# Kernel optimization log

Hardware: AMD Instinct MI355X
Metric: run time of the kernel (lower is better)

## Reference

```python
import math
import jax, jax.numpy as jnp
import numpy as np

L_LAYERS, H, D, DV, DM, LMAX, V = 4, 16, 1024, 64, 4096, 1024, 32000


def setup_inputs() -> dict:
    key = jax.random.key(0)
    ks = iter(jax.random.split(key, 40))
    def rn(shape, s=0.02):
        return jax.random.normal(next(ks), shape, jnp.float32) * s
    x_ids = jax.random.randint(next(ks), (LMAX,), 0, V)
    return dict(
        x_ids=x_ids,
        word_emb=rn((V, D)), pos_emb=rn((LMAX, D)),
        Wq=rn((L_LAYERS, H, D, D)), bq=jnp.zeros((L_LAYERS, H, D), jnp.float32),
        Wk=rn((L_LAYERS, H, D, D)), bk=jnp.zeros((L_LAYERS, H, D), jnp.float32),
        Wv=rn((L_LAYERS, H, D, DV)), bv=jnp.zeros((L_LAYERS, H, DV), jnp.float32),
        Wo=rn((L_LAYERS, H * DV, D)), bo=jnp.zeros((L_LAYERS, D), jnp.float32),
        g1=rn((L_LAYERS, D), 0.01), b1=rn((L_LAYERS, D), 0.01),
        g2=rn((L_LAYERS, D), 0.01), b2=rn((L_LAYERS, D), 0.01),
        W1=rn((L_LAYERS, D, DM)), bm1=jnp.zeros((L_LAYERS, DM), jnp.float32),
        W2=rn((L_LAYERS, DM, D)), bm2=jnp.zeros((L_LAYERS, D), jnp.float32),
        gf=rn((D,), 0.01), bf=rn((D,), 0.01),
        Wu=rn((D, V)), bu=jnp.zeros((V,), jnp.float32),
    )


def _ln(x, g, b):
    # original normalizes each row over the full embedding vector (biased std)
    mu = jnp.mean(x, axis=-1, keepdims=True)
    sd = jnp.sqrt(jnp.mean((x - mu) ** 2, axis=-1, keepdims=True))
    return g * (x - mu) / sd + b


def reference(x_ids, word_emb, pos_emb, Wq, bq, Wk, bk, Wv, bv, Wo, bo,
              g1, b1, g2, b2, W1, bm1, W2, bm2, gf, bf, Wu, bu):
    x = word_emb[x_ids] + pos_emb[jnp.arange(LMAX)]          # (LMAX, D)
    mask = jnp.tril(jnp.ones((LMAX, LMAX), bool))
    scale = 1.0 / math.sqrt(D)                               # d_attn = d_e
    for l in range(L_LAYERS):
        xn = _ln(x, g1[l], b1[l])
        q = jnp.einsum('ld,hde->hle', xn, Wq[l]) + bq[l][:, None, :]
        k = jnp.einsum('ld,hde->hle', xn, Wk[l]) + bk[l][:, None, :]
        v = jnp.einsum('ld,hdv->hlv', xn, Wv[l]) + bv[l][:, None, :]
        s = jnp.einsum('hqe,hke->hqk', q, k)                 # (H, LMAX, LMAX)
        s = jnp.where(mask, s, -jnp.inf)
        a = jax.nn.softmax(s * scale, axis=-1)
        o = jnp.einsum('hqk,hkv->hqv', a, v)                 # (H, LMAX, DV)
        # faithful reproduction of MHAttention's OVERLAPPING slice writes:
        # head h writes columns [h, h+DV), later heads overwrite earlier ones
        y = jnp.zeros((LMAX, H * DV), x.dtype)
        for h in range(H):
            y = y.at[:, h:h + DV].set(o[h])
        x = x + y @ Wo[l] + bo[l]
        xn2 = _ln(x, g2[l], b2[l])
        # x + act_layer(xn2) where act_layer(z) = z + mlp2(gelu(mlp1(z)))
        x = x + xn2 + jax.nn.gelu(xn2 @ W1[l] + bm1[l]) @ W2[l] + bm2[l]
    x = _ln(x, gf, bf)
    return jax.nn.softmax(x @ Wu + bu, axis=-1)              # (LMAX, V)
```

## Files before the change

### kernel.cpp

```cpp
#include <hip/hip_runtime.h>

typedef __bf16 bf16_t;
typedef __bf16 bf16x8 __attribute__((ext_vector_type(8)));
typedef float f32x4 __attribute__((ext_vector_type(4)));
typedef unsigned int u32;

#define SEQ    1024
#define DEMB   1024
#define NHEAD  16
#define DVDIM  64
#define DMLP   4096
#define NVOCAB 32000
#define NLAYER 4

typedef const __attribute__((address_space(1))) void gas_t;
typedef __attribute__((address_space(3))) void las_t;

__device__ __forceinline__ void gload_lds16(const void* g, void* l) {
  __builtin_amdgcn_global_load_lds((gas_t*)g, (las_t*)l, 16, 0, 0);
}

union PackU { bf16_t h[2]; u32 u; };
union B4U  { uint2 u; bf16_t h[4]; };

__device__ __forceinline__ float blockSum(float v, float* red) {
  #pragma unroll
  for (int o = 32; o > 0; o >>= 1) v += __shfl_down(v, o, 64);
  __syncthreads();
  if ((threadIdx.x & 63) == 0) red[threadIdx.x >> 6] = v;
  __syncthreads();
  return (red[0] + red[1]) + (red[2] + red[3]);
}
__device__ __forceinline__ float blockMax(float v, float* red) {
  #pragma unroll
  for (int o = 32; o > 0; o >>= 1) v = fmaxf(v, __shfl_down(v, o, 64));
  __syncthreads();
  if ((threadIdx.x & 63) == 0) red[threadIdx.x >> 6] = v;
  __syncthreads();
  return fmaxf(fmaxf(red[0], red[1]), fmaxf(red[2], red[3]));
}

__device__ __forceinline__ void ln_body(float4 v, const float* __restrict__ g,
                                        const float* __restrict__ b,
                                        bf16_t* __restrict__ xn, int row, int t,
                                        float* red, float* xupd_row) {
  float mu = blockSum(v.x + v.y + v.z + v.w, red) * (1.0f / DEMB);
  float dx = v.x - mu, dy = v.y - mu, dz = v.z - mu, dw = v.w - mu;
  float var = blockSum(dx * dx + dy * dy + dz * dz + dw * dw, red) * (1.0f / DEMB);
  float inv = 1.0f / sqrtf(var);
  float4 gv = *(const float4*)(g + t * 4);
  float4 bv = *(const float4*)(b + t * 4);
  float o0 = gv.x * dx * inv + bv.x;
  float o1 = gv.y * dy * inv + bv.y;
  float o2 = gv.z * dz * inv + bv.z;
  float o3 = gv.w * dw * inv + bv.w;
  PackU p0, p1;
  p0.h[0] = (bf16_t)o0; p0.h[1] = (bf16_t)o1;
  p1.h[0] = (bf16_t)o2; p1.h[1] = (bf16_t)o3;
  uint2 st; st.x = p0.u; st.y = p1.u;
  *(uint2*)(xn + (long)row * DEMB + t * 4) = st;
  if (xupd_row) {
    float4 nv; nv.x = v.x + o0; nv.y = v.y + o1; nv.z = v.z + o2; nv.w = v.w + o3;
    *(float4*)(xupd_row + t * 4) = nv;
  }
}

__global__ void __launch_bounds__(256)
embedln_k(const int* __restrict__ ids, const float* __restrict__ we,
          const float* __restrict__ pe, const float* __restrict__ g,
          const float* __restrict__ b, float* __restrict__ x,
          bf16_t* __restrict__ xn) {
  __shared__ float red[4];
  const int row = blockIdx.x, t = threadIdx.x;
  const long id = ids[row];
  float4 a = *(const float4*)(we + id * (long)DEMB + t * 4);
  float4 p = *(const float4*)(pe + (long)row * DEMB + t * 4);
  float4 v; v.x = a.x + p.x; v.y = a.y + p.y; v.z = a.z + p.z; v.w = a.w + p.w;
  *(float4*)(x + (long)row * DEMB + t * 4) = v;
  ln_body(v, g, b, xn, row, t, red, nullptr);
}

__global__ void __launch_bounds__(256)
ln_k(const float* __restrict__ x, const float* __restrict__ g,
     const float* __restrict__ b, bf16_t* __restrict__ xn,
     float* __restrict__ xupd) {
  __shared__ float red[4];
  const int row = blockIdx.x, t = threadIdx.x;
  float4 v = *(const float4*)(x + (long)row * DEMB + t * 4);
  ln_body(v, g, b, xn, row, t, red, xupd ? xupd + (long)row * DEMB : nullptr);
}

__global__ void __launch_bounds__(256)
redln_k(const float* __restrict__ P, const float* __restrict__ bm2,
        float* __restrict__ X, const float* __restrict__ g,
        const float* __restrict__ b, bf16_t* __restrict__ xn) {
  __shared__ float red[4];
  const int row = blockIdx.x, t = threadIdx.x;
  const long i = (long)row * 1024 + t * 4;
  float4 x = *(float4*)(X + i);
  #pragma unroll
  for (int z = 0; z < 4; ++z) {
    float4 p = *(const float4*)(P + (long)z * 1048576 + i);
    x.x += p.x; x.y += p.y; x.z += p.z; x.w += p.w;
  }
  float4 bb = *(const float4*)(bm2 + t * 4);
  x.x += bb.x; x.y += bb.y; x.z += bb.z; x.w += bb.w;
  *(float4*)(X + i) = x;
  ln_body(x, g, b, xn, row, t, red, nullptr);
}

__global__ void biaszyb_k(const float* __restrict__ bq, const float* __restrict__ bk,
                          float* __restrict__ out, bf16_t* __restrict__ y) {
  const int z = blockIdx.x, t = threadIdx.x;
  if (z < 128) {
    const int l = z >> 5, i = z & 31;
    const float* src = (i < NHEAD) ? (bq + (long)(l * NHEAD + i) * DEMB)
                                   : (bk + (long)(l * NHEAD + i - NHEAD) * DEMB);
    *(float4*)(out + (long)z * DEMB + t * 4) = *(const float4*)(src + t * 4);
  } else {
    *(uint4*)((char*)y + ((long)(z - 128) * 256 + t) * 16) = uint4{0, 0, 0, 0};
  }
}

__device__ __forceinline__ void tconv_tile(const float* __restrict__ ip,
                                           bf16_t* __restrict__ op,
                                           int R, int C, int rx, int ry,
                                           float (*tf)[65]) {
  const int c0 = rx * 64, r0 = ry * 64;
  const int t = threadIdx.x;
  const int lr = t >> 4, lc = (t & 15) * 4;
  #pragma unroll
  for (int p = 0; p < 4; ++p) {
    const float4 v = *(const float4*)(ip + (long)(r0 + lr + 16 * p) * C + (c0 + lc));
    tf[lr + 16 * p][lc + 0] = v.x;
    tf[lr + 16 * p][lc + 1] = v.y;
    tf[lr + 16 * p][lc + 2] = v.z;
    tf[lr + 16 * p][lc + 3] = v.w;
  }
  __syncthreads();
  const int j = t & 7;
  const int n = t >> 3;
  #pragma unroll
  for (int p = 0; p < 2; ++p) {
    const int nn = n + 32 * p;
    u32 w[4];
    #pragma unroll
    for (int q = 0; q < 4; ++q) {
      PackU u;
      u.h[0] = (bf16_t)tf[j * 8 + 2 * q][nn];
      u.h[1] = (bf16_t)tf[j * 8 + 2 * q + 1][nn];
      w[q] = u.u;
    }
    *(uint4*)(op + (long)(c0 + nn) * R + (r0 + j * 8)) = *(uint4*)&w[0];
  }
}

__global__ void __launch_bounds__(256)
tconvall_k(const float* __restrict__ Wq, const float* __restrict__ Wk,
           const float* __restrict__ Wv, const float* __restrict__ Wo,
           const float* __restrict__ W1, const float* __restrict__ W2,
           const float* __restrict__ Wu,
           bf16_t* __restrict__ WTqk, bf16_t* __restrict__ WTv,
           bf16_t* __restrict__ WTo, bf16_t* __restrict__ WT1,
           bf16_t* __restrict__ WT2, bf16_t* __restrict__ WTu) {
  __shared__ float tf[64][65];
  const long DD = (long)DEMB * DEMB;
  const int b = blockIdx.x;
  const float* ip; bf16_t* op; int R, C, rx, ry;
  if (b < 32768) {
    const int z = b >> 8, rem = b & 255; ry = rem >> 4; rx = rem & 15;
    R = 1024; C = 1024;
    const int l = z >> 5, i = z & 31;
    ip = (i < NHEAD) ? (Wq + (long)(l * NHEAD + i) * DD)
                     : (Wk + (long)(l * NHEAD + i - NHEAD) * DD);
    op = WTqk + (long)z * DD;
  } else if (b < 33792) {
    const int idx = b - 32768; const int z = idx >> 4; ry = idx & 15; rx = 0;
    R = 1024; C = 64;
    ip = Wv + (long)z * 65536; op = WTv + (long)z * 65536;
  } else if (b < 33920) {
    const int idx = b - 33792; const int z = idx >> 5; ry = (idx >> 4) & 1; rx = idx & 15;
    R = 128; C = 1024;
    ip = Wo + (long)z * DD; op = WTo + (long)z * 131072;
  } else if (b < 38016) {
    const int idx = b - 33920; const int z = idx >> 10; ry = (idx >> 6) & 15; rx = idx & 63;
    R = 1024; C = 4096;
    ip = W1 + (long)z * 4194304; op = WT1 + (long)z * 4194304;
  } else if (b < 42112) {
    const int idx = b - 38016; const int z = idx >> 10; ry = (idx >> 4) & 63; rx = idx & 15;
    R = 4096; C = 1024;
    ip = W2 + (long)z * 4194304; op = WT2 + (long)z * 4194304;
  } else {
    const int idx = b - 42112; ry = idx / 500; rx = idx - ry * 500;
    R = 1024; C = 32000;
    ip = Wu; op = WTu;
  }
  tconv_tile(ip, op, R, C, rx, ry, tf);
}

template<int MODE, int BN, bool CAUSAL, bool TRIMK>
__global__ void __launch_bounds__(256)
gemm_k(const bf16_t* __restrict__ A, const bf16_t* __restrict__ B,
       const float* __restrict__ bias, void* __restrict__ Cv,
       int M, int N, int K, int lda, int ldb,
       long aB, long bB, long cB, int biasB) {
  __shared__ bf16_t lsA[128 * 32];
  __shared__ bf16_t lsB[BN * 32];

  const int t = threadIdx.x;
  const int bz = blockIdx.z;
  const int m0 = blockIdx.y * 128;
  const int n0 = blockIdx.x * BN;
  if (CAUSAL && n0 > m0 + 127) return;

  const bf16_t* Ap = A + (long)bz * aB;
  const bf16_t* Bp = B + (long)bz * bB;
  const int kEnd = TRIMK ? min(K, m0 + 128) : K;

  constexpr int NS = BN / 32;
  const int lane = t & 63;
  const int wid = t >> 6;
  const int wr = (wid >> 1) * 64;
  const int wc = (wid & 1) * (BN / 2);
  const int fr = lane & 15, fg = lane >> 4;
  const int srow = lane >> 2;
  const int skc  = (lane & 3) * 8;

  f32x4 acc[4][NS] = {};

  for (int k0 = 0; k0 < kEnd; k0 += 32) {
    if (k0) __syncthreads();
    #pragma unroll
    for (int i = 0; i < 2; ++i) {
      const int seg = wid * 2 + i;
      gload_lds16(Ap + (long)(m0 + seg * 16 + srow) * lda + (k0 + skc),
                  lsA + seg * 512);
    }
    if (BN == 128) {
      #pragma unroll
      for (int i = 0; i < 2; ++i) {
        const int seg = wid * 2 + i;
        gload_lds16(Bp + (long)(n0 + seg * 16 + srow) * ldb + (k0 + skc),
                    lsB + seg * 512);
      }
    } else {
      gload_lds16(Bp + (long)(n0 + wid * 16 + srow) * ldb + (k0 + skc),
                  lsB + wid * 512);
    }
    __syncthreads();

    bf16x8 af[4], bfv[NS];
    #pragma unroll
    for (int ms = 0; ms < 4; ++ms)
      af[ms] = *(const bf16x8*)(lsA + (wr + ms * 16 + fr) * 32 + fg * 8);
    #pragma unroll
    for (int ns = 0; ns < NS; ++ns)
      bfv[ns] = *(const bf16x8*)(lsB + (wc + ns * 16 + fr) * 32 + fg * 8);
    #pragma unroll
    for (int ms = 0; ms < 4; ++ms)
      #pragma unroll
      for (int ns = 0; ns < NS; ++ns)
        acc[ms][ns] = __builtin_amdgcn_mfma_f32_16x16x32_bf16(
            af[ms], bfv[ns], acc[ms][ns], 0, 0, 0);
  }

  #pragma unroll
  for (int ms = 0; ms < 4; ++ms) {
    #pragma unroll
    for (int ns = 0; ns < NS; ++ns) {
      const int col = n0 + wc + ns * 16 + fr;
      const float bvv = bias ? bias[(long)bz * biasB + col] : 0.0f;
      #pragma unroll
      for (int r = 0; r < 4; ++r) {
        const int row = m0 + wr + ms * 16 + fg * 4 + r;
        float v = acc[ms][ns][r] + bvv;
        if (MODE == 1) {
          ((float*)Cv)[(long)bz * cB + (long)row * N + col] += v;
        } else if (MODE == 2) {
          ((float*)Cv)[(long)bz * cB + (long)row * N + col] = v;
        } else if (MODE == 3) {
          float gl = 0.5f * v * (1.0f + tanhf(0.7978845608028654f * (v + 0.044715f * v * v * v)));
          ((bf16_t*)Cv)[(long)bz * cB + (long)row * N + col] = (bf16_t)gl;
        } else {
          ((bf16_t*)Cv)[(long)row * 128 + 15 + col] = (bf16_t)v;
        }
      }
    }
  }
}

#define GPHASE(buf, mh, nh, STAGE, VM) do {                                            \
  bf16x8 af[4][2], bfv[2][2];                                                          \
  _Pragma("unroll") for (int mf = 0; mf < 4; ++mf) {                                   \
    const int r = wm * 128 + ((mh) * 4 + mf) * 16 + (lane & 15);                       \
    _Pragma("unroll") for (int ks = 0; ks < 2; ++ks) {                                 \
      const int slot = ks * 4 + (lane >> 4);                                           \
      af[mf][ks] = *(const bf16x8*)(lds + (buf) * 32768 + r * 64 +                     \
                                    ((slot ^ (r & 7)) << 3)); } }                      \
  _Pragma("unroll") for (int nf = 0; nf < 2; ++nf) {                                   \
    const int r = wn * 64 + ((nh) * 2 + nf) * 16 + (lane & 15);                        \
    _Pragma("unroll") for (int ks = 0; ks < 2; ++ks) {                                 \
      const int slot = ks * 4 + (lane >> 4);                                           \
      bfv[nf][ks] = *(const bf16x8*)(lds + (buf) * 32768 + 16384 + r * 64 +            \
                                     ((slot ^ (r & 7)) << 3)); } }                     \
  STAGE;                                                                               \
  __builtin_amdgcn_s_barrier();                                                        \
  asm volatile("s_waitcnt lgkmcnt(0)" ::: "memory");                                   \
  __builtin_amdgcn_sched_barrier(0);                                                   \
  __builtin_amdgcn_s_setprio(1);                                                       \
  _Pragma("unroll") for (int mf = 0; mf < 4; ++mf)                                     \
    _Pragma("unroll") for (int nf = 0; nf < 2; ++nf)                                   \
      _Pragma("unroll") for (int ks = 0; ks < 2; ++ks)                                 \
        acc[(mh) * 4 + mf][(nh) * 2 + nf] = __builtin_amdgcn_mfma_f32_16x16x32_bf16(   \
            af[mf][ks], bfv[nf][ks], acc[(mh) * 4 + mf][(nh) * 2 + nf], 0, 0, 0);      \
  __builtin_amdgcn_s_setprio(0);                                                       \
  VM;                                                                                  \
  __builtin_amdgcn_s_barrier();                                                        \
} while (0)

template<int MODE, bool CAUSAL, bool HASV>
__global__ void __launch_bounds__(512, 1)
gemm256_k(const bf16_t* __restrict__ A, const bf16_t* __restrict__ B,
          const float* __restrict__ bias, void* __restrict__ Cv,
          int M, int N, int K, long aB, long bB, long cB, int biasB,
          const bf16_t* __restrict__ B2, const float* __restrict__ bias2,
          bf16_t* __restrict__ Cv2) {
  __shared__ bf16_t lds[65536];

  const int t = threadIdx.x;
  const int lane = t & 63, w = t >> 6;
  const int wm = w >> 2, wn = w & 3;
  const int bz = blockIdx.z;
  const int m0 = blockIdx.y * 256, n0 = blockIdx.x * 256;
  if (CAUSAL && n0 > m0 + 255) return;

  const bool vm = HASV && (bz == 32);
  const bf16_t* Ap = A + (long)bz * aB;
  const bf16_t* Bp = vm ? B2 : B + (long)bz * bB;
  const int NT = K >> 6;

  f32x4 acc[8][4] = {};

  auto stA = [&](int half, int kt, int buf) {
    #pragma unroll
    for (int rr = 0; rr < 2; ++rr) {
      const int rw0 = rr * 64 + w * 8;
      const int row0 = ((rw0 >> 6) << 7) | (half << 6) | (rw0 & 63);
      const int r = row0 + (lane >> 3);
      const int slot = lane & 7;
      gload_lds16(Ap + (long)(m0 + r) * K + (kt << 6) + ((slot ^ (r & 7)) << 3),
                  lds + buf * 32768 + row0 * 64);
    }
  };
  auto stB = [&](int half, int kt, int buf) {
    #pragma unroll
    for (int rr = 0; rr < 2; ++rr) {
      const int rw0 = rr * 64 + w * 8;
      const int row0 = ((rw0 >> 5) << 6) | (half << 5) | (rw0 & 31);
      const int r = row0 + (lane >> 3);
      const int slot = lane & 7;
      gload_lds16(Bp + (long)(n0 + r) * K + (kt << 6) + ((slot ^ (r & 7)) << 3),
                  lds + buf * 32768 + 16384 + row0 * 64);
    }
  };

  stB(0, 0, 0); stA(0, 0, 0); stA(1, 0, 0); stB(1, 0, 0);
  stB(0, 1, 1); stA(0, 1, 1);
  asm volatile("s_waitcnt vmcnt(4)" ::: "memory");
  __builtin_amdgcn_s_barrier();

  for (int it = 0; it < (NT >> 1); ++it) {
    const int tt = it * 2;
    const int s1 = min(tt + 1, NT - 1);
    const int s2 = min(tt + 2, NT - 1);
    const int s3 = min(tt + 3, NT - 1);
    GPHASE(0, 0, 0, { stA(1, s1, 1); }, );
    GPHASE(0, 1, 0, { stB(1, s1, 1); }, );
    GPHASE(0, 0, 1, { stB(0, s2, 0); }, );
    GPHASE(0, 1, 1, { stA(0, s2, 0); }, asm volatile("s_waitcnt vmcnt(4)" ::: "memory"));
    GPHASE(1, 0, 0, { stA(1, s2, 0); }, );
    GPHASE(1, 1, 0, { stB(1, s2, 0); }, );
    GPHASE(1, 0, 1, { stB(0, s3, 1); }, );
    GPHASE(1, 1, 1, { stA(0, s3, 1); }, asm volatile("s_waitcnt vmcnt(4)" ::: "memory"));
  }
  asm volatile("s_waitcnt vmcnt(0)" ::: "memory");

  #pragma unroll
  for (int mf = 0; mf < 8; ++mf) {
    #pragma unroll
    for (int nf = 0; nf < 4; ++nf) {
      const int col = n0 + wn * 64 + nf * 16 + (lane & 15);
      const int row0 = m0 + wm * 128 + mf * 16 + (lane >> 4) * 4;
      if (HASV && vm) {
        const float bvv = bias2[col];
        PackU p0, p1;
        p0.h[0] = (bf16_t)(acc[mf][nf][0] + bvv);
        p0.h[1] = (bf16_t)(acc[mf][nf][1] + bvv);
        p1.h[0] = (bf16_t)(acc[mf][nf][2] + bvv);
        p1.h[1] = (bf16_t)(acc[mf][nf][3] + bvv);
        uint2 st; st.x = p0.u; st.y = p1.u;
        *(uint2*)(Cv2 + (long)col * M + row0) = st;
      } else {
        const float bvv = bias ? bias[(long)bz * biasB + col] : 0.0f;
        #pragma unroll
        for (int r = 0; r < 4; ++r) {
          const float v = acc[mf][nf][r] + bvv;
          if (MODE == 0)
            ((bf16_t*)Cv)[(long)bz * cB + (long)(row0 + r) * N + col] = (bf16_t)v;
          else
            ((float*)Cv)[(long)bz * cB + (long)(row0 + r) * N + col] = v;
        }
      }
    }
  }
}

__global__ void __launch_bounds__(256)
smax_k(bf16_t* __restrict__ s, const bf16_t* __restrict__ V,
       bf16_t* __restrict__ Yb) {
  __shared__ float red[4];
  const int q = blockIdx.x, h = blockIdx.y, t = threadIdx.x;
  bf16_t* sr = s + ((long)h * SEQ + q) * SEQ;
  const int L = q + 1;
  const float scale = 0.03125f;
  B4U b; b.u = *(const uint2*)(sr + t * 4);
  float x[4];
  float m = -1e30f;
  #pragma unroll
  for (int j = 0; j < 4; ++j) {
    x[j] = (float)b.h[j] * scale;
    if (t * 4 + j < L) m = fmaxf(m, x[j]);
  }
  m = blockMax(m, red);
  float e[4], sum = 0.0f;
  #pragma unroll
  for (int j = 0; j < 4; ++j) {
    e[j] = (t * 4 + j < L) ? expf(x[j] - m) : 0.0f;
    sum += e[j];
  }
  __syncthreads();
  sum = blockSum(sum, red);
  const float inv = 1.0f / sum;
  #pragma unroll
  for (int j = 0; j < 4; ++j) b.h[j] = (bf16_t)(e[j] * inv);
  *(uint2*)(sr + t * 4) = b.u;
  if (h != NHEAD - 1) {
    const bf16_t* vc = V + (long)h * 64 * SEQ;
    B4U vv; vv.u = *(const uint2*)(vc + t * 4);
    float d = 0.0f;
    #pragma unroll
    for (int j = 0; j < 4; ++j) d += e[j] * (float)vv.h[j];
    d = blockSum(d, red);
    if (t == 0) Yb[(long)q * 128 + h] = (bf16_t)(d * inv);
  }
}

__global__ void __launch_bounds__(1024)
vsmax_k(float* __restrict__ out) {
  __shared__ float rm[16], rs[16];
  const int row = blockIdx.x, t = threadIdx.x;
  float* r = out + (long)row * NVOCAB;
  float v[32];
  const int nlast = (t < NVOCAB - 31 * 1024) ? 32 : 31;
  float m = -1e30f;
  #pragma unroll
  for (int j = 0; j < 31; ++j) { v[j] = r[j * 1024 + t]; m = fmaxf(m, v[j]); }
  if (nlast == 32) { v[31] = r[31 * 1024 + t]; m = fmaxf(m, v[31]); } else v[31] = -1e30f;
  float s = 0.0f;
  #pragma unroll
  for (int j = 0; j < 32; ++j) s += expf(v[j] - m);
  #pragma unroll
  for (int o = 32; o > 0; o >>= 1) {
    const float mo = __shfl_down(m, o, 64);
    const float so = __shfl_down(s, o, 64);
    const float M2 = fmaxf(m, mo);
    s = s * expf(m - M2) + so * expf(mo - M2);
    m = M2;
  }
  if ((t & 63) == 0) { rm[t >> 6] = m; rs[t >> 6] = s; }
  __syncthreads();
  float M = -1e30f;
  #pragma unroll
  for (int i = 0; i < 16; ++i) M = fmaxf(M, rm[i]);
  float S = 0.0f;
  #pragma unroll
  for (int i = 0; i < 16; ++i) S += rs[i] * expf(rm[i] - M);
  const float inv = 1.0f / S;
  #pragma unroll
  for (int j = 0; j < 31; ++j) r[j * 1024 + t] = expf(v[j] - M) * inv;
  if (nlast == 32) r[31 * 1024 + t] = expf(v[31] - M) * inv;
}

extern "C" void kernel_launch(void* const* d_in, const int* in_sizes, int n_in,
                              void* d_out, int out_size, void* d_ws, size_t ws_size,
                              hipStream_t stream) {
  (void)in_sizes; (void)n_in; (void)out_size; (void)ws_size;
  const int*   x_ids = (const int*)  d_in[0];
  const float* wemb  = (const float*)d_in[1];
  const float* pemb  = (const float*)d_in[2];
  const float* Wq    = (const float*)d_in[3];
  const float* bq    = (const float*)d_in[4];
  const float* Wk    = (const float*)d_in[5];
  const float* bk    = (const float*)d_in[6];
  const float* Wv    = (const float*)d_in[7];
  const float* bv    = (const float*)d_in[8];
  const float* Wo    = (const float*)d_in[9];
  const float* bo    = (const float*)d_in[10];
  const float* g1    = (const float*)d_in[11];
  const float* b1    = (const float*)d_in[12];
  const float* g2    = (const float*)d_in[13];
  const float* b2    = (const float*)d_in[14];
  const float* W1    = (const float*)d_in[15];
  const float* bm1   = (const float*)d_in[16];
  const float* W2    = (const float*)d_in[17];
  const float* bm2   = (const float*)d_in[18];
  const float* gf    = (const float*)d_in[19];
  const float* bfin  = (const float*)d_in[20];
  const float* Wu    = (const float*)d_in[21];
  const float* bu    = (const float*)d_in[22];

  char* ws = (char*)d_ws;
  float*  X    = (float*) ws;
  bf16_t* ACT  = (bf16_t*)(ws + (4u   << 20));
  bf16_t* VbT  = (bf16_t*)(ws + (6u   << 20));
  bf16_t* Yb   = (bf16_t*)(ws + (10u  << 20));
  bf16_t* H1   = (bf16_t*)(ws + (12u  << 20));
  bf16_t* QKb  = (bf16_t*)(ws + (20u  << 20));
  float*  PART = (float*) (ws + (84u  << 20));
  float*  BIAS = (float*) (ws + (100u << 20));
  bf16_t* WTqk = (bf16_t*)(ws + (128u << 20));
  bf16_t* WTv  = (bf16_t*)(ws + (384u << 20));
  bf16_t* WTo  = (bf16_t*)(ws + (392u << 20));
  bf16_t* WT1  = (bf16_t*)(ws + (400u << 20));
  bf16_t* WT2  = (bf16_t*)(ws + (432u << 20));
  bf16_t* WTu  = (bf16_t*)(ws + (464u << 20));

  bf16_t* Sb  = (bf16_t*)d_out;
  float*  OUT = (float*)d_out;

  const long DD = (long)DEMB * DEMB;
  const long SD = (long)SEQ * DEMB;

  embedln_k<<<SEQ, 256, 0, stream>>>(x_ids, wemb, pemb, g1, b1, X, ACT);
  biaszyb_k<<<192, 256, 0, stream>>>(bq, bk, BIAS, Yb);
  tconvall_k<<<50112, 256, 0, stream>>>(Wq, Wk, Wv, Wo, W1, W2, Wu,
                                        WTqk, WTv, WTo, WT1, WT2, WTu);

  for (int l = 0; l < NLAYER; ++l) {
    gemm256_k<0, false, true><<<dim3(4, 4, 33), 512, 0, stream>>>(
        ACT, WTqk + (long)l * 32 * DD, BIAS + (long)l * 32 * DEMB, QKb,
        SEQ, DEMB, DEMB, 0L, DD, SD, DEMB,
        WTv + (long)l * DD, bv + (long)l * NHEAD * DVDIM, VbT);

    gemm256_k<0, true, false><<<dim3(4, 4, NHEAD), 512, 0, stream>>>(
        QKb, QKb + (long)NHEAD * SD, nullptr, Sb,
        SEQ, SEQ, DEMB, SD, SD, (long)SEQ * SEQ, 0, nullptr, nullptr, nullptr);
    smax_k<<<dim3(SEQ, NHEAD), 256, 0, stream>>>(Sb, VbT, Yb);
    gemm_k<7, 64, false, true><<<dim3(1, 8, 1), 256, 0, stream>>>(
        Sb + (long)(NHEAD - 1) * SEQ * SEQ, VbT + (long)(NHEAD - 1) * DVDIM * SEQ,
        nullptr, Yb, SEQ, DVDIM, SEQ, SEQ, SEQ, 0L, 0L, 0L, 0);

    gemm_k<1, 64, false, false><<<dim3(16, 8, 1), 256, 0, stream>>>(
        Yb, WTo + (long)l * DEMB * 128, bo + (long)l * DEMB, X,
        SEQ, DEMB, 128, 128, 128, 0L, 0L, 0L, 0);

    ln_k<<<SEQ, 256, 0, stream>>>(X, g2 + l * DEMB, b2 + l * DEMB, ACT, X);

    gemm_k<3, 128, false, false><<<dim3(32, 8, 1), 256, 0, stream>>>(
        ACT, WT1 + (long)l * DMLP * DEMB, bm1 + (long)l * DMLP, H1,
        SEQ, DMLP, DEMB, DEMB, DEMB, 0L, 0L, 0L, 0);
    gemm_k<2, 128, false, false><<<dim3(8, 8, 4), 256, 0, stream>>>(
        H1, WT2 + (long)l * DEMB * DMLP, nullptr, PART,
        SEQ, DEMB, 1024, DMLP, DMLP, 1024L, 1024L, (long)SEQ * DEMB, 0);
    if (l < NLAYER - 1)
      redln_k<<<SEQ, 256, 0, stream>>>(PART, bm2 + (long)l * DEMB, X,
                                       g1 + (l + 1) * DEMB, b1 + (l + 1) * DEMB, ACT);
    else
      redln_k<<<SEQ, 256, 0, stream>>>(PART, bm2 + (long)l * DEMB, X, gf, bfin, ACT);
  }

  gemm256_k<2, false, false><<<dim3(125, 4, 1), 512, 0, stream>>>(
      ACT, WTu, bu, OUT, SEQ, NVOCAB, DEMB, 0L, 0L, 0L, 0,
      nullptr, nullptr, nullptr);
  vsmax_k<<<SEQ, 1024, 0, stream>>>(OUT);
}
```

Before: 1.510 ms.

## Fold last-head PV into softmax and move V projection into score GEMM

The V projection moves out of the QK projection GEMM and becomes an extra z-slice of the causal score GEMM, which fills idle blocks left by the causal skip. The last head's full P·V product, previously a separate small GEMM, is now computed inside the softmax kernel using LDS-staged probabilities, and the normalized probabilities are no longer written back to the score buffer. This removes one kernel launch and a large write of softmax output, at the cost of a heavier per-row loop in the last-head softmax blocks.

```diff
diff --git a/kernel.cpp b/kernel.cpp
--- a/kernel.cpp
+++ b/kernel.cpp
@@ -278,11 +278,9 @@
           ((float*)Cv)[(long)bz * cB + (long)row * N + col] += v;
         } else if (MODE == 2) {
           ((float*)Cv)[(long)bz * cB + (long)row * N + col] = v;
-        } else if (MODE == 3) {
+        } else {
           float gl = 0.5f * v * (1.0f + tanhf(0.7978845608028654f * (v + 0.044715f * v * v * v)));
           ((bf16_t*)Cv)[(long)bz * cB + (long)row * N + col] = (bf16_t)gl;
-        } else {
-          ((bf16_t*)Cv)[(long)row * 128 + 15 + col] = (bf16_t)v;
         }
       }
     }
@@ -318,13 +316,13 @@
   __builtin_amdgcn_s_barrier();                                                        \
 } while (0)
 
-template<int MODE, bool CAUSAL, bool HASV>
+template<int MODE, bool CAUSAL, int VZ>
 __global__ void __launch_bounds__(512, 1)
 gemm256_k(const bf16_t* __restrict__ A, const bf16_t* __restrict__ B,
           const float* __restrict__ bias, void* __restrict__ Cv,
           int M, int N, int K, long aB, long bB, long cB, int biasB,
-          const bf16_t* __restrict__ B2, const float* __restrict__ bias2,
-          bf16_t* __restrict__ Cv2) {
+          const bf16_t* __restrict__ A2, const bf16_t* __restrict__ B2,
+          const float* __restrict__ bias2, bf16_t* __restrict__ Cv2) {
   __shared__ bf16_t lds[65536];
 
   const int t = threadIdx.x;
@@ -332,10 +330,10 @@
   const int wm = w >> 2, wn = w & 3;
   const int bz = blockIdx.z;
   const int m0 = blockIdx.y * 256, n0 = blockIdx.x * 256;
-  if (CAUSAL && n0 > m0 + 255) return;
-
-  const bool vm = HASV && (bz == 32);
-  const bf16_t* Ap = A + (long)bz * aB;
+  const bool vm = (VZ >= 0) && (bz == VZ);
+  if (CAUSAL && !vm && n0 > m0 + 255) return;
+
+  const bf16_t* Ap = vm ? A2 : A + (long)bz * aB;
   const bf16_t* Bp = vm ? B2 : B + (long)bz * bB;
   const int NT = K >> 6;
 
@@ -391,7 +389,7 @@
     for (int nf = 0; nf < 4; ++nf) {
       const int col = n0 + wn * 64 + nf * 16 + (lane & 15);
       const int row0 = m0 + wm * 128 + mf * 16 + (lane >> 4) * 4;
-      if (HASV && vm) {
+      if (vm) {
         const float bvv = bias2[col];
         PackU p0, p1;
         p0.h[0] = (bf16_t)(acc[mf][nf][0] + bvv);
@@ -416,11 +414,13 @@
 }
 
 __global__ void __launch_bounds__(256)
-smax_k(bf16_t* __restrict__ s, const bf16_t* __restrict__ V,
+smax_k(const bf16_t* __restrict__ s, const bf16_t* __restrict__ V,
        bf16_t* __restrict__ Yb) {
   __shared__ float red[4];
+  __shared__ float pl[1024];
+  __shared__ float rcol[4][64];
   const int q = blockIdx.x, h = blockIdx.y, t = threadIdx.x;
-  bf16_t* sr = s + ((long)h * SEQ + q) * SEQ;
+  const bf16_t* sr = s + ((long)h * SEQ + q) * SEQ;
   const int L = q + 1;
   const float scale = 0.03125f;
   B4U b; b.u = *(const uint2*)(sr + t * 4);
@@ -441,17 +441,34 @@
   __syncthreads();
   sum = blockSum(sum, red);
   const float inv = 1.0f / sum;
-  #pragma unroll
-  for (int j = 0; j < 4; ++j) b.h[j] = (bf16_t)(e[j] * inv);
-  *(uint2*)(sr + t * 4) = b.u;
   if (h != NHEAD - 1) {
     const bf16_t* vc = V + (long)h * 64 * SEQ;
     B4U vv; vv.u = *(const uint2*)(vc + t * 4);
     float d = 0.0f;
     #pragma unroll
     for (int j = 0; j < 4; ++j) d += e[j] * (float)vv.h[j];
+    __syncthreads();
     d = blockSum(d, red);
     if (t == 0) Yb[(long)q * 128 + h] = (bf16_t)(d * inv);
+  } else {
+    #pragma unroll
+    for (int j = 0; j < 4; ++j) pl[t * 4 + j] = e[j];
+    __syncthreads();
+    const int c = t & 63, grp = t >> 6;
+    const bf16_t* vr = V + ((long)(NHEAD - 1) * 64 + c) * SEQ + grp * 256;
+    float part = 0.0f;
+    #pragma unroll
+    for (int kk = 0; kk < 256; kk += 8) {
+      bf16x8 v8 = *(const bf16x8*)(vr + kk);
+      #pragma unroll
+      for (int j = 0; j < 8; ++j) part += pl[grp * 256 + kk + j] * (float)v8[j];
+    }
+    rcol[grp][c] = part;
+    __syncthreads();
+    if (t < 64) {
+      const float d = rcol[0][t] + rcol[1][t] + rcol[2][t] + rcol[3][t];
+      Yb[(long)q * 128 + 15 + t] = (bf16_t)(d * inv);
+    }
   }
 }
 
@@ -547,18 +564,17 @@
                                         WTqk, WTv, WTo, WT1, WT2, WTu);
 
   for (int l = 0; l < NLAYER; ++l) {
-    gemm256_k<0, false, true><<<dim3(4, 4, 33), 512, 0, stream>>>(
+    gemm256_k<0, false, -1><<<dim3(4, 4, 32), 512, 0, stream>>>(
         ACT, WTqk + (long)l * 32 * DD, BIAS + (long)l * 32 * DEMB, QKb,
         SEQ, DEMB, DEMB, 0L, DD, SD, DEMB,
-        WTv + (long)l * DD, bv + (long)l * NHEAD * DVDIM, VbT);
-
-    gemm256_k<0, true, false><<<dim3(4, 4, NHEAD), 512, 0, stream>>>(
+        nullptr, nullptr, nullptr, nullptr);
+
+    gemm256_k<0, true, NHEAD><<<dim3(4, 4, NHEAD + 1), 512, 0, stream>>>(
         QKb, QKb + (long)NHEAD * SD, nullptr, Sb,
-        SEQ, SEQ, DEMB, SD, SD, (long)SEQ * SEQ, 0, nullptr, nullptr, nullptr);
+        SEQ, SEQ, DEMB, SD, SD, (long)SEQ * SEQ, 0,
+        ACT, WTv + (long)l * DD, bv + (long)l * NHEAD * DVDIM, VbT);
+
     smax_k<<<dim3(SEQ, NHEAD), 256, 0, stream>>>(Sb, VbT, Yb);
-    gemm_k<7, 64, false, true><<<dim3(1, 8, 1), 256, 0, stream>>>(
-        Sb + (long)(NHEAD - 1) * SEQ * SEQ, VbT + (long)(NHEAD - 1) * DVDIM * SEQ,
-        nullptr, Yb, SEQ, DVDIM, SEQ, SEQ, SEQ, 0L, 0L, 0L, 0);
 
     gemm_k<1, 64, false, false><<<dim3(16, 8, 1), 256, 0, stream>>>(
         Yb, WTo + (long)l * DEMB * 128, bo + (long)l * DEMB, X,
@@ -579,8 +595,8 @@
       redln_k<<<SEQ, 256, 0, stream>>>(PART, bm2 + (long)l * DEMB, X, gf, bfin, ACT);
   }
 
-  gemm256_k<2, false, false><<<dim3(125, 4, 1), 512, 0, stream>>>(
+  gemm256_k<2, false, -1><<<dim3(125, 4, 1), 512, 0, stream>>>(
       ACT, WTu, bu, OUT, SEQ, NVOCAB, DEMB, 0L, 0L, 0L, 0,
-      nullptr, nullptr, nullptr);
+      nullptr, nullptr, nullptr, nullptr);
   vsmax_k<<<SEQ, 1024, 0, stream>>>(OUT);
 }
```

Result: no change. 1.503 ms (-0.5%).
